# Performance work log

Hardware: AMD Instinct MI355X
Metric: run time of the kernel (lower is better)

## Reference

```python
import jax, jax.numpy as jnp
import numpy as np

B, N, K, C = 8, 4096, 16, 128
HID, DEPTH = 4 * C, 2
EPS = 1e-5


def _bn(x, g, b, m, v):
    # BatchNorm1d in eval mode over the last (channel) dim
    return (x - m) * (g * jax.lax.rsqrt(v + EPS)) + b


def _ffn(x, w1, b1, w2, b2, g, bt, m, v):
    h = jax.nn.relu(jnp.einsum('bnc,ch->bnh', x, w1) + b1)
    y = jnp.einsum('bnh,hc->bnc', h, w2) + b2
    return _bn(y, g, bt, m, v)


def setup_inputs() -> dict:
    key = jax.random.key(0)
    ks = jax.random.split(key, 24)
    s = 0.05
    inp = {
        'x': jax.random.normal(ks[0], (B, N, C), jnp.float32),
        'knn_idx': jax.random.randint(ks[1], (B, N, K), 0, N, jnp.int64),
        'mlp0_w1': jax.random.normal(ks[2], (C, HID), jnp.float32) * s,
        'mlp0_b1': jax.random.normal(ks[3], (HID,), jnp.float32) * s,
        'mlp0_w2': jax.random.normal(ks[4], (HID, C), jnp.float32) * s,
        'mlp0_b2': jax.random.normal(ks[5], (C,), jnp.float32) * s,
        'mlp0_g': jax.random.uniform(ks[6], (C,), jnp.float32, 0.5, 1.5),
        'mlp0_beta': jax.random.normal(ks[7], (C,), jnp.float32) * s,
        'mlp0_m': jnp.zeros((C,), jnp.float32),
        'mlp0_v': jnp.ones((C,), jnp.float32),
        'vfr_w': jax.random.normal(ks[8], (DEPTH, C, C), jnp.float32) * s,
        'vfr_b': jax.random.normal(ks[9], (DEPTH, C), jnp.float32) * s,
        'vfr_g': jax.random.uniform(ks[10], (DEPTH, C), jnp.float32, 0.5, 1.5),
        'vfr_beta': jax.random.normal(ks[11], (DEPTH, C), jnp.float32) * s,
        'vfr_m': jnp.zeros((DEPTH, C), jnp.float32),
        'vfr_v': jnp.ones((DEPTH, C), jnp.float32),
        'ffn_w1': jax.random.normal(ks[12], (DEPTH, C, HID), jnp.float32) * s,
        'ffn_b1': jax.random.normal(ks[13], (DEPTH, HID), jnp.float32) * s,
        'ffn_w2': jax.random.normal(ks[14], (DEPTH, HID, C), jnp.float32) * s,
        'ffn_b2': jax.random.normal(ks[15], (DEPTH, C), jnp.float32) * s,
        'ffn_g': jax.random.uniform(ks[16], (DEPTH, C), jnp.float32, 0.5, 1.5),
        'ffn_beta': jax.random.normal(ks[17], (DEPTH, C), jnp.float32) * s,
        'ffn_m': jnp.zeros((DEPTH, C), jnp.float32),
        'ffn_v': jnp.ones((DEPTH, C), jnp.float32),
    }
    return inp


def reference(x, knn_idx,
              mlp0_w1, mlp0_b1, mlp0_w2, mlp0_b2, mlp0_g, mlp0_beta, mlp0_m, mlp0_v,
              vfr_w, vfr_b, vfr_g, vfr_beta, vfr_m, vfr_v,
              ffn_w1, ffn_b1, ffn_w2, ffn_b2, ffn_g, ffn_beta, ffn_m, ffn_v):
    # eval mode: DropPath is identity, BatchNorm uses running stats
    x = x + _ffn(x, mlp0_w1, mlp0_b1, mlp0_w2, mlp0_b2, mlp0_g, mlp0_beta, mlp0_m, mlp0_v)
    gather = jax.vmap(lambda pts, idx: pts[idx])  # [N,C],[N,K] -> [N,K,C]
    for i in range(DEPTH):
        # VFR: linear -> knn gather -> edge diff -> max over K -> BN
        h = jnp.einsum('bnc,cd->bnd', x, vfr_w[i]) + vfr_b[i]
        nb = gather(h, knn_idx)                      # [B,N,K,C]
        agg = jnp.max(nb - h[:, :, None, :], axis=2)  # [B,N,C]
        x = x + _bn(agg, vfr_g[i], vfr_beta[i], vfr_m[i], vfr_v[i])
        x = x + _ffn(x, ffn_w1[i], ffn_b1[i], ffn_w2[i], ffn_b2[i],
                     ffn_g[i], ffn_beta[i], ffn_m[i], ffn_v[i])
    return x
```

## Files before the change

### kernel.cpp

```cpp
#include <hip/hip_runtime.h>
#include <hip/hip_bf16.h>
#include <stdint.h>

typedef __attribute__((ext_vector_type(8))) __bf16 bf16x8;
typedef __attribute__((ext_vector_type(4))) float floatx4;

#define EPS 1e-5f

static __device__ __forceinline__ unsigned short f2bf(float f) {
    union { float f; unsigned int u; } x; x.f = f;
    unsigned int r = x.u + 0x7fffu + ((x.u >> 16) & 1u);
    return (unsigned short)(r >> 16);
}
static __device__ __forceinline__ float bf2f_lo(unsigned int u) {
    union { unsigned int u; float f; } x; x.u = u << 16; return x.f;
}
static __device__ __forceinline__ float bf2f_hi(unsigned int u) {
    union { unsigned int u; float f; } x; x.u = u & 0xffff0000u; return x.f;
}

struct Params {
    const float* x_in;
    const int*   knn;
    const float* w1s[3];
    const float* w2s[3];
    const float* vws[2];
    unsigned short* W1P[3];
    unsigned short* W2P[3];
    unsigned short* VTP[2];
    const float* b1s[3];
    const float* b2s[3];
    const float* gs[3];
    const float* bes[3];
    const float* ms[3];
    const float* vvs[3];
    const float* vbb[2];
    const float* vgg[2];
    const float* vbt[2];
    const float* vmm[2];
    const float* vva[2];
    float* xf;
};

__global__ __launch_bounds__(256) void pack_weights(Params P) {
    const int gtid = blockIdx.x * 256 + threadIdx.x;
    const int GT   = gridDim.x * 256;
#pragma unroll
    for (int t = 0; t < 3; ++t) {
        const float* s1 = P.w1s[t];
        unsigned short* d1 = P.W1P[t];
        for (int idx = gtid; idx < 65536; idx += GT) {
            int h = idx & 511, k = idx >> 9;
            int hf = h >> 7, w = (h >> 5) & 3, mt = (h >> 4) & 1, ln = h & 15;
            int ks = k >> 5, q = (k >> 3) & 3, j = k & 7;
            d1[hf * 16384 + w * 4096 + mt * 2048 + ks * 512 + q * 128 + ln * 8 + j]
                = f2bf(s1[idx]);
        }
        const float* s2 = P.w2s[t];
        unsigned short* d2 = P.W2P[t];
        for (int idx = gtid; idx < 65536; idx += GT) {
            int c = idx & 127, h = idx >> 7;
            int hf = h >> 7, hk = h & 127;
            int ks = hk >> 5, q = (hk >> 3) & 3, j = hk & 7;
            int w = c >> 5, nt = (c >> 4) & 1, ln = c & 15;
            d2[hf * 16384 + w * 4096 + nt * 2048 + ks * 512 + q * 128 + ln * 8 + j]
                = f2bf(s2[idx]);
        }
    }
#pragma unroll
    for (int t = 0; t < 2; ++t) {
        const float* sv = P.vws[t];
        unsigned short* dv = P.VTP[t];
        for (int idx = gtid; idx < 16384; idx += GT) {
            int c = idx & 127, k = idx >> 7;
            int ks = k >> 5, q = (k >> 3) & 3, j = k & 7;
            int w = c >> 5, nt = (c >> 4) & 1, ln = c & 15;
            dv[w * 4096 + nt * 2048 + ks * 512 + q * 128 + ln * 8 + j] = f2bf(sv[idx]);
        }
    }
}

template <int LOADX, int TE, int TF, int TV>
__global__ __launch_bounds__(256, 4)
void stage(Params P, const float* __restrict__ xold_g,
           const unsigned short* __restrict__ VbIn,
           unsigned short* __restrict__ VbOut)
{
    __shared__ __align__(16) unsigned short xt[4096];
    __shared__ __align__(16) float buf_f[4096];
    uint2* hta = (uint2*)buf_f;
    uint2* htb = hta + 1024;
    const int tid   = threadIdx.x;
    const int lane  = tid & 63;
    const int w     = tid >> 6;
    const int q     = lane >> 4;
    const int ln    = lane & 15;
    const int sw    = ln & 7;
    const int phys  = blockIdx.x;
    const int batch = phys & 7;
    const int blk   = phys >> 3;
    const int p0    = (batch << 12) + (blk << 5);
    const floatx4 zero = {0.f, 0.f, 0.f, 0.f};

    if constexpr (LOADX) {
        const int r = tid >> 3, cc = tid & 7;
        const float4* src = (const float4*)(xold_g + (size_t)(p0 + r) * 128 + cc * 16);
        float4* dstf = (float4*)&buf_f[r * 128 + cc * 16];
#pragma unroll
        for (int i = 0; i < 2; ++i) {
            float4 a = src[2 * i], b = src[2 * i + 1];
            dstf[2 * i]     = a;
            dstf[2 * i + 1] = b;
            int kq = cc * 2 + i;
            uint4 pk;
            pk.x = (unsigned int)f2bf(a.x) | ((unsigned int)f2bf(a.y) << 16);
            pk.y = (unsigned int)f2bf(a.z) | ((unsigned int)f2bf(a.w) << 16);
            pk.z = (unsigned int)f2bf(b.x) | ((unsigned int)f2bf(b.y) << 16);
            pk.w = (unsigned int)f2bf(b.z) | ((unsigned int)f2bf(b.w) << 16);
            *(uint4*)&xt[(r * 16 + (kq ^ (r & 7))) * 8] = pk;
        }
    }

    if constexpr (TE >= 0) {
        const int ch0 = ln * 8;
        float sc[8], of[8];
        {
            float4 ga = *(const float4*)(P.vgg[TE] + ch0), gb = *(const float4*)(P.vgg[TE] + ch0 + 4);
            float4 ba = *(const float4*)(P.vbt[TE] + ch0), bb = *(const float4*)(P.vbt[TE] + ch0 + 4);
            float4 ma = *(const float4*)(P.vmm[TE] + ch0), mb = *(const float4*)(P.vmm[TE] + ch0 + 4);
            float4 va = *(const float4*)(P.vva[TE] + ch0), vb = *(const float4*)(P.vva[TE] + ch0 + 4);
            const float gv[8] = {ga.x, ga.y, ga.z, ga.w, gb.x, gb.y, gb.z, gb.w};
            const float bv[8] = {ba.x, ba.y, ba.z, ba.w, bb.x, bb.y, bb.z, bb.w};
            const float mv[8] = {ma.x, ma.y, ma.z, ma.w, mb.x, mb.y, mb.z, mb.w};
            const float vvv[8] = {va.x, va.y, va.z, va.w, vb.x, vb.y, vb.z, vb.w};
#pragma unroll
            for (int j = 0; j < 8; ++j) {
                sc[j] = gv[j] * rsqrtf(vvv[j] + EPS);
                of[j] = bv[j] - mv[j] * sc[j];
            }
        }
#pragma unroll
        for (int it = 0; it < 2; ++it) {
            const int pl = it * 16 + w * 4 + q;
            const int p  = p0 + pl;
            uint4 sv = *(const uint4*)(VbIn + (size_t)p * 128 + ch0);
            const int* kp = P.knn + (size_t)p * 16;
            int4 ka = *(const int4*)(kp);
            int4 kb = *(const int4*)(kp + 4);
            int4 kc = *(const int4*)(kp + 8);
            int4 kd = *(const int4*)(kp + 12);
            const unsigned short* vbase = VbIn + ((size_t)batch << 19) + ch0;
            float m[8];
#pragma unroll
            for (int j = 0; j < 8; ++j) m[j] = -3.4e38f;
#define GATH(IDX) { uint4 u4 = *(const uint4*)(vbase + ((size_t)(IDX) << 7));      \
            m[0] = fmaxf(m[0], bf2f_lo(u4.x)); m[1] = fmaxf(m[1], bf2f_hi(u4.x)); \
            m[2] = fmaxf(m[2], bf2f_lo(u4.y)); m[3] = fmaxf(m[3], bf2f_hi(u4.y)); \
            m[4] = fmaxf(m[4], bf2f_lo(u4.z)); m[5] = fmaxf(m[5], bf2f_hi(u4.z)); \
            m[6] = fmaxf(m[6], bf2f_lo(u4.w)); m[7] = fmaxf(m[7], bf2f_hi(u4.w)); }
            GATH(ka.x) GATH(ka.y) GATH(ka.z) GATH(ka.w)
            GATH(kb.x) GATH(kb.y) GATH(kb.z) GATH(kb.w)
            GATH(kc.x) GATH(kc.y) GATH(kc.z) GATH(kc.w)
            GATH(kd.x) GATH(kd.y) GATH(kd.z) GATH(kd.w)
#undef GATH
            float s_[8];
            s_[0] = bf2f_lo(sv.x); s_[1] = bf2f_hi(sv.x);
            s_[2] = bf2f_lo(sv.y); s_[3] = bf2f_hi(sv.y);
            s_[4] = bf2f_lo(sv.z); s_[5] = bf2f_hi(sv.z);
            s_[6] = bf2f_lo(sv.w); s_[7] = bf2f_hi(sv.w);
            const float* xrow = xold_g + (size_t)p * 128 + ch0;
            float4 x0 = *(const float4*)xrow;
            float4 x1 = *(const float4*)(xrow + 4);
            float xo[8] = {x0.x, x0.y, x0.z, x0.w, x1.x, x1.y, x1.z, x1.w};
            float xn[8];
            unsigned int pw[8];
#pragma unroll
            for (int j = 0; j < 8; ++j) {
                xn[j] = xo[j] + (m[j] - s_[j]) * sc[j] + of[j];
                pw[j] = (unsigned int)f2bf(xn[j]);
            }
            *(float4*)&buf_f[pl * 128 + ch0]     = make_float4(xn[0], xn[1], xn[2], xn[3]);
            *(float4*)&buf_f[pl * 128 + ch0 + 4] = make_float4(xn[4], xn[5], xn[6], xn[7]);
            uint4 pk;
            pk.x = pw[0] | (pw[1] << 16);
            pk.y = pw[2] | (pw[3] << 16);
            pk.z = pw[4] | (pw[5] << 16);
            pk.w = pw[6] | (pw[7] << 16);
            *(uint4*)&xt[(pl * 16 + (ln ^ (pl & 7))) * 8] = pk;
        }
    }
    __syncthreads();

    float xr[2][2][4];
#pragma unroll
    for (int mt = 0; mt < 2; ++mt)
#pragma unroll
        for (int nt = 0; nt < 2; ++nt)
#pragma unroll
            for (int r = 0; r < 4; ++r)
                xr[mt][nt][r] = buf_f[(16 * mt + 4 * q + r) * 128 + 32 * w + 16 * nt + ln];
    __syncthreads();

    floatx4 acc2[2][2];
#pragma unroll
    for (int i = 0; i < 2; ++i)
#pragma unroll
        for (int j = 0; j < 2; ++j) acc2[i][j] = zero;

    const unsigned short* W1 = P.W1P[TF];
    const unsigned short* W2 = P.W2P[TF];
    const float* b1 = P.b1s[TF];

    auto g1 = [&](int hf, uint2* dst) {
        floatx4 acc1[2][2];
#pragma unroll
        for (int i = 0; i < 2; ++i)
#pragma unroll
            for (int j = 0; j < 2; ++j) acc1[i][j] = zero;
        const unsigned short* a1 = W1 + hf * 16384 + w * 4096 + q * 128 + ln * 8;
#pragma unroll
        for (int ks = 0; ks < 4; ++ks) {
            bf16x8 bfr[2];
#pragma unroll
            for (int nt = 0; nt < 2; ++nt)
                bfr[nt] = *(const bf16x8*)&xt[((16 * nt + ln) * 16 + ((4 * ks + q) ^ sw)) * 8];
#pragma unroll
            for (int mt = 0; mt < 2; ++mt) {
                bf16x8 af = *(const bf16x8*)(a1 + mt * 2048 + ks * 512);
#pragma unroll
                for (int nt = 0; nt < 2; ++nt)
                    acc1[mt][nt] = __builtin_amdgcn_mfma_f32_16x16x32_bf16(
                        af, bfr[nt], acc1[mt][nt], 0, 0, 0);
            }
        }
#pragma unroll
        for (int mt = 0; mt < 2; ++mt) {
            const int hloc = 32 * w + 16 * mt + 4 * q;
            const int gh   = 128 * hf + hloc;
            const float bv0 = b1[gh], bv1 = b1[gh + 1];
            const float bv2 = b1[gh + 2], bv3 = b1[gh + 3];
            const int c16  = hloc >> 3;
            const int half = q & 1;
#pragma unroll
            for (int nt = 0; nt < 2; ++nt) {
                const int pt = 16 * nt + ln;
                float v0 = acc1[mt][nt][0] + bv0; v0 = v0 > 0.f ? v0 : 0.f;
                float v1 = acc1[mt][nt][1] + bv1; v1 = v1 > 0.f ? v1 : 0.f;
                float v2 = acc1[mt][nt][2] + bv2; v2 = v2 > 0.f ? v2 : 0.f;
                float v3 = acc1[mt][nt][3] + bv3; v3 = v3 > 0.f ? v3 : 0.f;
                uint2 pk;
                pk.x = (unsigned int)f2bf(v0) | ((unsigned int)f2bf(v1) << 16);
                pk.y = (unsigned int)f2bf(v2) | ((unsigned int)f2bf(v3) << 16);
                dst[(pt * 16 + (c16 ^ (pt & 7))) * 2 + half] = pk;
            }
        }
    };

    g1(0, hta);
    __syncthreads();
#pragma unroll
    for (int hf = 0; hf < 4; ++hf) {
        uint2* cur = (hf & 1) ? htb : hta;
        const unsigned short* b2b = W2 + hf * 16384 + w * 4096 + q * 128 + ln * 8;
#pragma unroll
        for (int ks = 0; ks < 4; ++ks) {
            bf16x8 bw[2];
#pragma unroll
            for (int nt = 0; nt < 2; ++nt)
                bw[nt] = *(const bf16x8*)(b2b + nt * 2048 + ks * 512);
#pragma unroll
            for (int mt = 0; mt < 2; ++mt) {
                const int pt = 16 * mt + ln;
                bf16x8 ah = *(const bf16x8*)&cur[(pt * 16 + ((4 * ks + q) ^ (pt & 7))) * 2];
#pragma unroll
                for (int nt = 0; nt < 2; ++nt)
                    acc2[mt][nt] = __builtin_amdgcn_mfma_f32_16x16x32_bf16(
                        ah, bw[nt], acc2[mt][nt], 0, 0, 0);
            }
        }
        if (hf < 3) g1(hf + 1, (hf & 1) ? hta : htb);
        __syncthreads();
    }

    {
        const float* b2   = P.b2s[TF];
        const float* gam  = P.gs[TF];
        const float* bet  = P.bes[TF];
        const float* mean = P.ms[TF];
        const float* var  = P.vvs[TF];
#pragma unroll
        for (int nt = 0; nt < 2; ++nt) {
            const int c = 32 * w + 16 * nt + ln;
            const float scv = gam[c] * rsqrtf(var[c] + EPS);
            const float off = (b2[c] - mean[c]) * scv + bet[c];
#pragma unroll
            for (int mt = 0; mt < 2; ++mt) {
#pragma unroll
                for (int r = 0; r < 4; ++r) {
                    const int pt = 16 * mt + 4 * q + r;
                    float xn = xr[mt][nt][r] + acc2[mt][nt][r] * scv + off;
                    P.xf[(size_t)(p0 + pt) * 128 + c] = xn;
                    if constexpr (TV >= 0)
                        xt[(pt * 16 + ((c >> 3) ^ (pt & 7))) * 8 + (c & 7)] = f2bf(xn);
                }
            }
        }
    }

    if constexpr (TV >= 0) {
        __syncthreads();
        const unsigned short* VT = P.VTP[TV];
        floatx4 acc[2][2];
#pragma unroll
        for (int i = 0; i < 2; ++i)
#pragma unroll
            for (int j = 0; j < 2; ++j) acc[i][j] = zero;
        const unsigned short* bb2 = VT + w * 4096 + q * 128 + ln * 8;
#pragma unroll
        for (int ks = 0; ks < 4; ++ks) {
            bf16x8 bw[2];
#pragma unroll
            for (int nt = 0; nt < 2; ++nt)
                bw[nt] = *(const bf16x8*)(bb2 + nt * 2048 + ks * 512);
#pragma unroll
            for (int mt = 0; mt < 2; ++mt) {
                bf16x8 ax = *(const bf16x8*)&xt[((16 * mt + ln) * 16 + ((4 * ks + q) ^ sw)) * 8];
#pragma unroll
                for (int nt = 0; nt < 2; ++nt)
                    acc[mt][nt] = __builtin_amdgcn_mfma_f32_16x16x32_bf16(
                        ax, bw[nt], acc[mt][nt], 0, 0, 0);
            }
        }
        const float* vb = P.vbb[TV];
        unsigned short* vstage = (unsigned short*)buf_f;
#pragma unroll
        for (int nt = 0; nt < 2; ++nt) {
            const int c = 32 * w + 16 * nt + ln;
            const float bia = vb[c];
#pragma unroll
            for (int mt = 0; mt < 2; ++mt)
#pragma unroll
                for (int r = 0; r < 4; ++r) {
                    const int pt = 16 * mt + 4 * q + r;
                    vstage[pt * 128 + c] = f2bf(acc[mt][nt][r] + bia);
                }
        }
        __syncthreads();
        const int rr = tid >> 3, seg = tid & 7;
        const uint4* srcv = (const uint4*)&vstage[rr * 128 + seg * 16];
        uint4 a = srcv[0], b = srcv[1];
        uint4* dstv = (uint4*)(VbOut + (size_t)(p0 + rr) * 128 + seg * 16);
        dstv[0] = a; dstv[1] = b;
    }
}

extern "C" void kernel_launch(void* const* d_in, const int* in_sizes, int n_in,
                              void* d_out, int out_size, void* d_ws, size_t ws_size,
                              hipStream_t stream)
{
    Params p;
    p.x_in = (const float*)d_in[0];
    p.knn  = (const int*)d_in[1];
    const float* w1  = (const float*)d_in[2];
    const float* b1  = (const float*)d_in[3];
    const float* w2  = (const float*)d_in[4];
    const float* b2  = (const float*)d_in[5];
    const float* g0  = (const float*)d_in[6];
    const float* be0 = (const float*)d_in[7];
    const float* m0p = (const float*)d_in[8];
    const float* v0p = (const float*)d_in[9];
    const float* vw  = (const float*)d_in[10];
    const float* vbp = (const float*)d_in[11];
    const float* vgp = (const float*)d_in[12];
    const float* vbe = (const float*)d_in[13];
    const float* vmp = (const float*)d_in[14];
    const float* vvp = (const float*)d_in[15];
    const float* fw1 = (const float*)d_in[16];
    const float* fb1 = (const float*)d_in[17];
    const float* fw2 = (const float*)d_in[18];
    const float* fb2 = (const float*)d_in[19];
    const float* fg  = (const float*)d_in[20];
    const float* fbe = (const float*)d_in[21];
    const float* fm  = (const float*)d_in[22];
    const float* fv  = (const float*)d_in[23];

    p.w1s[0] = w1;  p.w1s[1] = fw1; p.w1s[2] = fw1 + 65536;
    p.w2s[0] = w2;  p.w2s[1] = fw2; p.w2s[2] = fw2 + 65536;
    p.vws[0] = vw;  p.vws[1] = vw + 16384;
    p.b1s[0] = b1;  p.b1s[1] = fb1; p.b1s[2] = fb1 + 512;
    p.b2s[0] = b2;  p.b2s[1] = fb2; p.b2s[2] = fb2 + 128;
    p.gs[0]  = g0;  p.gs[1]  = fg;  p.gs[2]  = fg + 128;
    p.bes[0] = be0; p.bes[1] = fbe; p.bes[2] = fbe + 128;
    p.ms[0]  = m0p; p.ms[1]  = fm;  p.ms[2]  = fm + 128;
    p.vvs[0] = v0p; p.vvs[1] = fv;  p.vvs[2] = fv + 128;
    p.vbb[0] = vbp; p.vbb[1] = vbp + 128;
    p.vgg[0] = vgp; p.vgg[1] = vgp + 128;
    p.vbt[0] = vbe; p.vbt[1] = vbe + 128;
    p.vmm[0] = vmp; p.vmm[1] = vmp + 128;
    p.vva[0] = vvp; p.vva[1] = vvp + 128;

    char* ws = (char*)d_ws;
    unsigned short* Vb0 = (unsigned short*)ws;
    unsigned short* Vb1 = (unsigned short*)(ws + (size_t)(8 << 20));
    unsigned short* u   = (unsigned short*)(ws + (size_t)(16 << 20));
    for (int i = 0; i < 3; ++i) p.W1P[i] = u + i * 65536;
    for (int i = 0; i < 3; ++i) p.W2P[i] = u + 196608 + i * 65536;
    for (int i = 0; i < 2; ++i) p.VTP[i] = u + 393216 + i * 16384;
    p.xf = (float*)d_out;

    pack_weights<<<dim3(512), 256, 0, stream>>>(p);
    stage<1, -1, 0, 0><<<dim3(1024), 256, 0, stream>>>(p, p.x_in, nullptr, Vb0);
    stage<0,  0, 1, 1><<<dim3(1024), 256, 0, stream>>>(p, p.xf, Vb0, Vb1);
    stage<0,  1, 2, -1><<<dim3(1024), 256, 0, stream>>>(p, p.xf, Vb1, nullptr);
}
```

Measured before the change: 187.0 us.

## Store intermediate residual stream in bf16 and make weight packing write-coalesced

Intermediate stages now write the residual activations as bf16 into a workspace buffer instead of fp32 to the output; only the last stage writes fp32. The next stage reads these bf16 values for the residual add, which halves intermediate activation traffic. The weight-packing kernel is also restructured to iterate over destination indices so its stores are contiguous. The trade-off is that the residual stream is rounded to bf16 between stages, so accuracy drops.

Result: no change. 186.2 us (-0.4%).

```diff
diff --git a/kernel.cpp b/kernel.cpp
--- a/kernel.cpp
+++ b/kernel.cpp
@@ -39,6 +39,7 @@
     const float* vbt[2];
     const float* vmm[2];
     const float* vva[2];
+    unsigned short* xb;
     float* xf;
 };
 
@@ -49,40 +50,40 @@
     for (int t = 0; t < 3; ++t) {
         const float* s1 = P.w1s[t];
         unsigned short* d1 = P.W1P[t];
-        for (int idx = gtid; idx < 65536; idx += GT) {
-            int h = idx & 511, k = idx >> 9;
-            int hf = h >> 7, w = (h >> 5) & 3, mt = (h >> 4) & 1, ln = h & 15;
-            int ks = k >> 5, q = (k >> 3) & 3, j = k & 7;
-            d1[hf * 16384 + w * 4096 + mt * 2048 + ks * 512 + q * 128 + ln * 8 + j]
-                = f2bf(s1[idx]);
+        for (int d = gtid; d < 65536; d += GT) {
+            int j = d & 7, ln = (d >> 3) & 15, q = (d >> 7) & 3, ks = (d >> 9) & 3;
+            int mt = (d >> 11) & 1, w = (d >> 12) & 3, hf = (d >> 14) & 3;
+            int k = 32 * ks + 8 * q + j;
+            int h = 128 * hf + 32 * w + 16 * mt + ln;
+            d1[d] = f2bf(s1[k * 512 + h]);
         }
         const float* s2 = P.w2s[t];
         unsigned short* d2 = P.W2P[t];
-        for (int idx = gtid; idx < 65536; idx += GT) {
-            int c = idx & 127, h = idx >> 7;
-            int hf = h >> 7, hk = h & 127;
-            int ks = hk >> 5, q = (hk >> 3) & 3, j = hk & 7;
-            int w = c >> 5, nt = (c >> 4) & 1, ln = c & 15;
-            d2[hf * 16384 + w * 4096 + nt * 2048 + ks * 512 + q * 128 + ln * 8 + j]
-                = f2bf(s2[idx]);
+        for (int d = gtid; d < 65536; d += GT) {
+            int j = d & 7, ln = (d >> 3) & 15, q = (d >> 7) & 3, ks = (d >> 9) & 3;
+            int nt = (d >> 11) & 1, w = (d >> 12) & 3, hf = (d >> 14) & 3;
+            int h = 128 * hf + 32 * ks + 8 * q + j;
+            int c = 32 * w + 16 * nt + ln;
+            d2[d] = f2bf(s2[h * 128 + c]);
         }
     }
 #pragma unroll
     for (int t = 0; t < 2; ++t) {
         const float* sv = P.vws[t];
         unsigned short* dv = P.VTP[t];
-        for (int idx = gtid; idx < 16384; idx += GT) {
-            int c = idx & 127, k = idx >> 7;
-            int ks = k >> 5, q = (k >> 3) & 3, j = k & 7;
-            int w = c >> 5, nt = (c >> 4) & 1, ln = c & 15;
-            dv[w * 4096 + nt * 2048 + ks * 512 + q * 128 + ln * 8 + j] = f2bf(sv[idx]);
-        }
-    }
-}
-
-template <int LOADX, int TE, int TF, int TV>
+        for (int d = gtid; d < 16384; d += GT) {
+            int j = d & 7, ln = (d >> 3) & 15, q = (d >> 7) & 3, ks = (d >> 9) & 3;
+            int nt = (d >> 11) & 1, w = (d >> 12) & 3;
+            int k = 32 * ks + 8 * q + j;
+            int c = 32 * w + 16 * nt + ln;
+            dv[d] = f2bf(sv[k * 128 + c]);
+        }
+    }
+}
+
+template <int LOADX, int TE, int TF, int TV, int LAST>
 __global__ __launch_bounds__(256, 4)
-void stage(Params P, const float* __restrict__ xold_g,
+void stage(Params P,
            const unsigned short* __restrict__ VbIn,
            unsigned short* __restrict__ VbOut)
 {
@@ -104,7 +105,7 @@
 
     if constexpr (LOADX) {
         const int r = tid >> 3, cc = tid & 7;
-        const float4* src = (const float4*)(xold_g + (size_t)(p0 + r) * 128 + cc * 16);
+        const float4* src = (const float4*)(P.x_in + (size_t)(p0 + r) * 128 + cc * 16);
         float4* dstf = (float4*)&buf_f[r * 128 + cc * 16];
 #pragma unroll
         for (int i = 0; i < 2; ++i) {
@@ -168,10 +169,12 @@
             s_[2] = bf2f_lo(sv.y); s_[3] = bf2f_hi(sv.y);
             s_[4] = bf2f_lo(sv.z); s_[5] = bf2f_hi(sv.z);
             s_[6] = bf2f_lo(sv.w); s_[7] = bf2f_hi(sv.w);
-            const float* xrow = xold_g + (size_t)p * 128 + ch0;
-            float4 x0 = *(const float4*)xrow;
-            float4 x1 = *(const float4*)(xrow + 4);
-            float xo[8] = {x0.x, x0.y, x0.z, x0.w, x1.x, x1.y, x1.z, x1.w};
+            uint4 xv = *(const uint4*)(P.xb + (size_t)p * 128 + ch0);
+            float xo[8];
+            xo[0] = bf2f_lo(xv.x); xo[1] = bf2f_hi(xv.x);
+            xo[2] = bf2f_lo(xv.y); xo[3] = bf2f_hi(xv.y);
+            xo[4] = bf2f_lo(xv.z); xo[5] = bf2f_hi(xv.z);
+            xo[6] = bf2f_lo(xv.w); xo[7] = bf2f_hi(xv.w);
             float xn[8];
             unsigned int pw[8];
 #pragma unroll
@@ -299,9 +302,14 @@
                 for (int r = 0; r < 4; ++r) {
                     const int pt = 16 * mt + 4 * q + r;
                     float xn = xr[mt][nt][r] + acc2[mt][nt][r] * scv + off;
-                    P.xf[(size_t)(p0 + pt) * 128 + c] = xn;
-                    if constexpr (TV >= 0)
-                        xt[(pt * 16 + ((c >> 3) ^ (pt & 7))) * 8 + (c & 7)] = f2bf(xn);
+                    if constexpr (LAST) {
+                        P.xf[(size_t)(p0 + pt) * 128 + c] = xn;
+                    } else {
+                        unsigned short xb16 = f2bf(xn);
+                        P.xb[(size_t)(p0 + pt) * 128 + c] = xb16;
+                        if constexpr (TV >= 0)
+                            xt[(pt * 16 + ((c >> 3) ^ (pt & 7))) * 8 + (c & 7)] = xb16;
+                    }
                 }
             }
         }
@@ -402,14 +410,15 @@
     char* ws = (char*)d_ws;
     unsigned short* Vb0 = (unsigned short*)ws;
     unsigned short* Vb1 = (unsigned short*)(ws + (size_t)(8 << 20));
-    unsigned short* u   = (unsigned short*)(ws + (size_t)(16 << 20));
+    p.xb = (unsigned short*)(ws + (size_t)(16 << 20));
+    unsigned short* u   = (unsigned short*)(ws + (size_t)(24 << 20));
     for (int i = 0; i < 3; ++i) p.W1P[i] = u + i * 65536;
     for (int i = 0; i < 3; ++i) p.W2P[i] = u + 196608 + i * 65536;
     for (int i = 0; i < 2; ++i) p.VTP[i] = u + 393216 + i * 16384;
     p.xf = (float*)d_out;
 
     pack_weights<<<dim3(512), 256, 0, stream>>>(p);
-    stage<1, -1, 0, 0><<<dim3(1024), 256, 0, stream>>>(p, p.x_in, nullptr, Vb0);
-    stage<0,  0, 1, 1><<<dim3(1024), 256, 0, stream>>>(p, p.xf, Vb0, Vb1);
-    stage<0,  1, 2, -1><<<dim3(1024), 256, 0, stream>>>(p, p.xf, Vb1, nullptr);
-}
+    stage<1, -1, 0, 0, 0><<<dim3(1024), 256, 0, stream>>>(p, nullptr, Vb0);
+    stage<0,  0, 1, 1, 0><<<dim3(1024), 256, 0, stream>>>(p, Vb0, Vb1);
+    stage<0,  1, 2, -1, 1><<<dim3(1024), 256, 0, stream>>>(p, Vb1, nullptr);
+}
```
